# Performance work log

Measured on AMD Instinct MI355X. Metric: run time of the kernel, lower is better.

The kernel has to match this reference:

```python
import jax, jax.numpy as jnp
import numpy as np

GROUPS = 8   # GroupNorm groups used by create_pat_conv*_blocks(..., groups=8)
EPS = 1e-5
K = 20       # num_neighbor


def group_norm(x, gamma, beta):
    # x: [B, C, ...spatial]
    B, C = x.shape[0], x.shape[1]
    shape = x.shape
    xg = x.reshape(B, GROUPS, C // GROUPS, -1)
    m = xg.mean(axis=(2, 3), keepdims=True)
    v = ((xg - m) ** 2).mean(axis=(2, 3), keepdims=True)
    xg = (xg - m) * jax.lax.rsqrt(v + EPS)
    x = xg.reshape(shape)
    bshape = (1, C) + (1,) * (len(shape) - 2)
    return x * gamma.reshape(bshape) + beta.reshape(bshape)


def conv_block(x, w, b, gamma, beta):
    # pointwise (kernel-size 1) conv + GroupNorm + ELU, works for 1d and 2d spatial
    y = jnp.einsum('oc,bc...->bo...', w, x) + b.reshape((1, -1) + (1,) * (x.ndim - 2))
    return jax.nn.elu(group_norm(y, gamma, beta))


def knn_graph(points, k):
    # points: [B, 3, N] -> neighbor coords [B, 3, N, k] (self included, dilation=1)
    sq = jnp.sum(points * points, axis=1)                      # [B, N]
    inner = jnp.einsum('bci,bcj->bij', points, points)         # [B, N, N]
    dist = sq[:, :, None] + sq[:, None, :] - 2.0 * inner       # squared pairwise dist
    _, idx = jax.lax.top_k(-dist, k)                           # [B, N, k] smallest dists
    neighbors = jnp.take_along_axis(points[:, :, None, :], idx[:, None, :, :], axis=3)
    return neighbors                                           # [B, 3, N, k]


def setup_inputs() -> dict:
    key = jax.random.key(0)
    B, N = 4, 8192
    dims1 = [6, 32, 64]
    dims2 = [64, 512, 1024]
    keys = iter(jax.random.split(key, 32))
    inp = {"points": jax.random.normal(next(keys), (B, 3, N), dtype=jnp.float32)}
    for tag, dims in (("p1", dims1), ("p2", dims2)):
        for i in range(len(dims) - 1):
            cin, cout = dims[i], dims[i + 1]
            inp[f"{tag}_w{i}"] = jax.random.normal(next(keys), (cout, cin), dtype=jnp.float32) / np.float32(np.sqrt(cin))
            inp[f"{tag}_b{i}"] = jnp.zeros((cout,), dtype=jnp.float32)
            inp[f"{tag}_g{i}"] = jnp.ones((cout,), dtype=jnp.float32)
            inp[f"{tag}_beta{i}"] = jnp.zeros((cout,), dtype=jnp.float32)
    return inp


def reference(points, p1_w0, p1_b0, p1_g0, p1_beta0, p1_w1, p1_b1, p1_g1, p1_beta1,
              p2_w0, p2_b0, p2_g0, p2_beta0, p2_w1, p2_b1, p2_g1, p2_beta1):
    neighbors = knn_graph(points, K)                             # [B, 3, N, K]
    center = jnp.broadcast_to(points[:, :, :, None], neighbors.shape)
    x = jnp.concatenate([center, neighbors - center], axis=1)   # [B, 6, N, K]
    x = conv_block(x, p1_w0, p1_b0, p1_g0, p1_beta0)            # [B, 32, N, K]
    x = conv_block(x, p1_w1, p1_b1, p1_g1, p1_beta1)            # [B, 64, N, K]
    x = jnp.max(x, axis=2)                                      # [B, 64, K] (faithful to source: max over dim=2)
    x = conv_block(x, p2_w0, p2_b0, p2_g0, p2_beta0)            # [B, 512, K]
    x = conv_block(x, p2_w1, p2_b1, p2_g1, p2_beta1)            # [B, 1024, K]
    return x
```

## Files before the change

### kernel.cpp

```cpp
#include <hip/hip_runtime.h>
#include <math.h>

#define NPTS   8192
#define BATCH  4
#define KNN    20
#define NKTOT  (NPTS*KNN)
#define EPS    1e-5f
#define TILE2  2048

typedef float v2f __attribute__((ext_vector_type(2)));

__device__ __forceinline__ float elu(float x) { return x > 0.0f ? x : expm1f(x); }
__device__ __forceinline__ float eluf(float x) { return x > 0.0f ? x : __expf(x) - 1.0f; }
__device__ __forceinline__ v2f splat2(float x) { v2f v; v.x = x; v.y = x; return v; }
__device__ __forceinline__ float rfl(float x) {
    return __uint_as_float(__builtin_amdgcn_readfirstlane(__float_as_uint(x)));
}

__device__ __forceinline__ unsigned fenc(float f) {
    unsigned b = __float_as_uint(f);
    return b ^ ((unsigned)(((int)b) >> 31) | 0x80000000u);
}
__device__ __forceinline__ float fdec(unsigned u) {
    unsigned b = (u & 0x80000000u) ? (u ^ 0x80000000u) : ~u;
    return __uint_as_float(b);
}

__global__ __launch_bounds__(256) void prep_kernel(const float* __restrict__ points,
                                                   float4* __restrict__ pts4)
{
    const int t = blockIdx.x * 256 + threadIdx.x;
    const int b = t >> 13, n = t & (NPTS - 1);
    const float* px = points + b * 3 * NPTS;
    float x = px[n], y = px[NPTS + n], z = px[2 * NPTS + n];
    pts4[t] = make_float4(x, y, z, -0.5f * (x * x + y * y + z * z));
}

__global__ __launch_bounds__(256, 4) void knn_kernel(const float4* __restrict__ pts4,
                                                     int* __restrict__ idx_out)
{
    __shared__ __align__(16) float4 tileS[TILE2];
    const int tid  = threadIdx.x;
    const int lane = tid & 63;
    const int wv   = tid >> 6;
    const int b    = blockIdx.x >> 8;
    const int q0   = (blockIdx.x & 255) * 32 + wv * 8;
    const float4* pb = pts4 + b * NPTS;

    float qx[8], qy[8], qz[8];
    v2f smax2[8];
#pragma unroll
    for (int q = 0; q < 8; ++q) {
        float4 qp = pb[q0 + q];
        qx[q] = rfl(qp.x); qy[q] = rfl(qp.y); qz[q] = rfl(qp.z);
        smax2[q] = splat2(-INFINITY);
    }

    for (int t = 0; t < NPTS / TILE2; ++t) {
        __syncthreads();
        for (int i = tid; i < TILE2; i += 256) tileS[i] = pb[t * TILE2 + i];
        __syncthreads();
#pragma unroll 4
        for (int s = 0; s < TILE2 / 128; ++s) {
            float4 p0 = tileS[s * 128 + lane];
            float4 p1 = tileS[s * 128 + 64 + lane];
            v2f px = { p0.x, p1.x }, py = { p0.y, p1.y };
            v2f pz = { p0.z, p1.z }, pw = { p0.w, p1.w };
#pragma unroll
            for (int q = 0; q < 8; ++q) {
                v2f sv = __builtin_elementwise_fma(splat2(qx[q]), px,
                         __builtin_elementwise_fma(splat2(qy[q]), py,
                         __builtin_elementwise_fma(splat2(qz[q]), pz, pw)));
                smax2[q] = __builtin_elementwise_max(smax2[q], sv);
            }
        }
    }

    float sgate[8];
#pragma unroll
    for (int q = 0; q < 8; ++q) {
        float v = fmaxf(smax2[q].x, smax2[q].y);
#pragma unroll
        for (int k = 2; k <= 64; k <<= 1)
#pragma unroll
            for (int j = k >> 1; j >= 1; j >>= 1) {
                float o = __shfl_xor(v, j);
                bool up = ((lane & k) == 0);
                bool keepmin = (((lane & j) == 0) == up);
                v = keepmin ? fminf(v, o) : fmaxf(v, o);
            }
        float m = __shfl(v, 44);
        sgate[q] = m - 1e-4f - 1e-5f * fabsf(m);
    }

    float mys[8]; int myi[8]; float scur[8];
#pragma unroll
    for (int q = 0; q < 8; ++q) { mys[q] = -INFINITY; myi[q] = -1; scur[q] = -INFINITY; }

    for (int t = 0; t < NPTS / TILE2; ++t) {
        __syncthreads();
        for (int i = tid; i < TILE2; i += 256) tileS[i] = pb[t * TILE2 + i];
        __syncthreads();
        for (int s = 0; s < TILE2 / 128; ++s) {
            float4 p0 = tileS[s * 128 + lane];
            float4 p1 = tileS[s * 128 + 64 + lane];
            v2f px = { p0.x, p1.x }, py = { p0.y, p1.y };
            v2f pz = { p0.z, p1.z }, pw = { p0.w, p1.w };
            v2f sv2[8];
#pragma unroll
            for (int q = 0; q < 8; ++q)
                sv2[q] = __builtin_elementwise_fma(splat2(qx[q]), px,
                         __builtin_elementwise_fma(splat2(qy[q]), py,
                         __builtin_elementwise_fma(splat2(qz[q]), pz, pw)));
            const int jb = t * TILE2 + s * 128;
#pragma unroll
            for (int q = 0; q < 8; ++q) {
#pragma unroll
                for (int h = 0; h < 2; ++h) {
                    float svh = h ? sv2[q].y : sv2[q].x;
                    unsigned long long bal = __ballot(svh >= sgate[q]);
                    while (bal) {
                        int src = __ffsll(bal) - 1;
                        bal &= bal - 1;
                        float vs = __shfl(svh, src);
                        int   vi = jb + h * 64 + src;
                        if (vs > scur[q]) {
                            int   sh = (mys[q] < vs) ? 1 : 0;
                            float pd = __shfl_up(mys[q], 1);
                            int   pi = __shfl_up(myi[q], 1);
                            int   ps = __shfl_up(sh, 1);
                            bool pshift = (lane > 0) && (ps != 0);
                            mys[q] = sh ? (pshift ? pd : vs) : mys[q];
                            myi[q] = sh ? (pshift ? pi : vi) : myi[q];
                            scur[q] = __shfl(mys[q], 19);
                        }
                    }
                }
            }
        }
    }

#pragma unroll
    for (int q = 0; q < 8; ++q) {
        const int qi = q0 + q;
        if (lane < KNN) idx_out[(b * NPTS + qi) * KNN + lane] = myi[q];
    }
}

__global__ __launch_bounds__(256) void moments_x_kernel(const float* __restrict__ points,
                                                        const int* __restrict__ idx,
                                                        float* __restrict__ sums1p)
{
    const int t = blockIdx.x * 256 + threadIdx.x;
    const int b = blockIdx.x / 640;
    const int r = t - b * NKTOT;
    const int n = r / KNN;
    const float* px = points + b * 3 * NPTS;
    const int j = idx[t];
    float cx = px[n], cy = px[NPTS + n], cz = px[2 * NPTS + n];
    float v[27];
    v[0] = cx; v[1] = cy; v[2] = cz;
    v[3] = px[j] - cx; v[4] = px[NPTS + j] - cy; v[5] = px[2 * NPTS + j] - cz;
    int p = 6;
#pragma unroll
    for (int d = 0; d < 6; ++d)
#pragma unroll
        for (int e = d; e < 6; ++e) v[p++] = v[d] * v[e];
#pragma unroll
    for (int i = 0; i < 27; ++i)
        for (int o = 32; o > 0; o >>= 1) v[i] += __shfl_xor(v[i], o);

    __shared__ float red[4][27];
    const int lane = threadIdx.x & 63, w = threadIdx.x >> 6;
    if (lane == 0)
#pragma unroll
        for (int i = 0; i < 27; ++i) red[w][i] = v[i];
    __syncthreads();
    if (threadIdx.x < 27) {
        float acc = red[0][threadIdx.x] + red[1][threadIdx.x] + red[2][threadIdx.x] + red[3][threadIdx.x];
        int slot = blockIdx.x & 63;
        atomicAdd(&sums1p[(slot * BATCH + b) * 27 + threadIdx.x], acc);
    }
}

__global__ void finalize1_kernel(const float* __restrict__ sums1p,
                                 const float* __restrict__ w1, const float* __restrict__ b1,
                                 const float* __restrict__ g1, const float* __restrict__ beta1,
                                 float* __restrict__ w1f)
{
    __shared__ float S[BATCH][27];
    const int t = threadIdx.x;
    if (t < 108) {
        int b = t / 27, i = t % 27;
        float acc = 0.f;
        for (int s = 0; s < 64; ++s) acc += sums1p[(s * BATCH + b) * 27 + i];
        S[b][i] = acc;
    }
    __syncthreads();
    const int b = t >> 5, c = t & 31;
    const float invS = 1.0f / (float)NKTOT;
    float Ex[6], M[6][6];
#pragma unroll
    for (int d = 0; d < 6; ++d) Ex[d] = S[b][d] * invS;
    int p = 6;
#pragma unroll
    for (int d = 0; d < 6; ++d)
#pragma unroll
        for (int e = d; e < 6; ++e) { float v = S[b][p++] * invS; M[d][e] = v; M[e][d] = v; }
    const int g = c >> 2;
    float msum = 0.f, qsum = 0.f;
    for (int cc = g * 4; cc < g * 4 + 4; ++cc) {
        float w[6];
#pragma unroll
        for (int d = 0; d < 6; ++d) w[d] = w1[cc * 6 + d];
        float dotEx = 0.f;
#pragma unroll
        for (int d = 0; d < 6; ++d) dotEx += w[d] * Ex[d];
        float Ey = dotEx + b1[cc];
        float Ey2 = 0.f;
#pragma unroll
        for (int d = 0; d < 6; ++d)
#pragma unroll
            for (int e = 0; e < 6; ++e) Ey2 += w[d] * w[e] * M[d][e];
        Ey2 += 2.0f * b1[cc] * dotEx + b1[cc] * b1[cc];
        msum += Ey; qsum += Ey2;
    }
    float m = msum * 0.25f;
    float var = qsum * 0.25f - m * m;
    float inv = rsqrtf(var + EPS);
    float s = g1[c] * inv;
    float tt = s * (b1[c] - m) + beta1[c];
    float* o = w1f + (b * 32 + c) * 8;
#pragma unroll
    for (int d = 0; d < 6; ++d) o[d] = s * w1[c * 6 + d];
    o[6] = tt; o[7] = 0.f;
}

__global__ __launch_bounds__(256, 5) void fused_main_kernel(
    const float4* __restrict__ pts4, const int* __restrict__ idxb,
    const float* __restrict__ w1f, const float* __restrict__ w2, const float* __restrict__ b2,
    float* __restrict__ sums2p, unsigned int* __restrict__ maxenc, unsigned int* __restrict__ minenc)
{
    __shared__ __align__(16) float w2t[32 * 64];
    __shared__ __align__(16) float z1s[32 * 64];
    __shared__ __align__(16) float4 w1s4[64];
    __shared__ float b2s[64];
    __shared__ float redmx[64], redmn[64], sqred[32];

    const int t   = threadIdx.x;
    const int blk = blockIdx.x;
    const int nc  = blk & 15;
    const int k   = (blk >> 4) % 20;
    const int b   = blk / 320;

    for (int i = t; i < 512; i += 256) {
        float4 v = ((const float4*)w2)[i];
        int c = i >> 3, kq = (i & 7) * 4;
        w2t[(kq + 0) * 64 + c] = v.x; w2t[(kq + 1) * 64 + c] = v.y;
        w2t[(kq + 2) * 64 + c] = v.z; w2t[(kq + 3) * 64 + c] = v.w;
    }
    if (t < 64) { w1s4[t] = ((const float4*)w1f)[b * 64 + t]; b2s[t] = b2[t]; }

    const int ln   = t & 63;
    const int cg   = t >> 6;
    const int pos0 = (t & 15) * 4;
    const int c0   = (t >> 4) * 4;
    const float4* pb = pts4 + b * NPTS;
    const int nbase = nc * 512;

    float mx[4], mn[4];
#pragma unroll
    for (int ci = 0; ci < 4; ++ci) { mx[ci] = -INFINITY; mn[ci] = INFINITY; }
    float gs = 0.f, gq = 0.f;

    for (int st = 0; st < 8; ++st) {
        const int n = nbase + st * 64 + ln;
        const int j = idxb[(b * NPTS + n) * KNN + k];
        float4 c4 = pb[n];
        float4 e4 = pb[j];
        float x0[6] = { c4.x, c4.y, c4.z, e4.x - c4.x, e4.y - c4.y, e4.z - c4.z };

        __syncthreads();
#pragma unroll
        for (int jj = 0; jj < 8; ++jj) {
            int c = cg * 8 + jj;
            float4 wA = w1s4[c * 2 + 0];
            float4 wB = w1s4[c * 2 + 1];
            float z = wB.z;
            z = fmaf(wA.x, x0[0], z); z = fmaf(wA.y, x0[1], z); z = fmaf(wA.z, x0[2], z);
            z = fmaf(wA.w, x0[3], z); z = fmaf(wB.x, x0[4], z); z = fmaf(wB.y, x0[5], z);
            z1s[c * 64 + ln] = eluf(z);
        }
        __syncthreads();

        float acc[4][4];
#pragma unroll
        for (int ci = 0; ci < 4; ++ci) {
            float bb = b2s[c0 + ci];
#pragma unroll
            for (int pj = 0; pj < 4; ++pj) acc[ci][pj] = bb;
        }
#pragma unroll
        for (int kk = 0; kk < 32; ++kk) {
            float4 av = *(const float4*)&w2t[kk * 64 + c0];
            float4 bv = *(const float4*)&z1s[kk * 64 + pos0];
            float avv[4] = { av.x, av.y, av.z, av.w };
            float bvv[4] = { bv.x, bv.y, bv.z, bv.w };
#pragma unroll
            for (int ci = 0; ci < 4; ++ci)
#pragma unroll
                for (int pj = 0; pj < 4; ++pj) acc[ci][pj] = fmaf(avv[ci], bvv[pj], acc[ci][pj]);
        }
#pragma unroll
        for (int ci = 0; ci < 4; ++ci)
#pragma unroll
            for (int pj = 0; pj < 4; ++pj) {
                float v = acc[ci][pj];
                gs += v; gq = fmaf(v, v, gq);
                mx[ci] = fmaxf(mx[ci], v); mn[ci] = fminf(mn[ci], v);
            }
    }

#pragma unroll
    for (int m = 1; m <= 8; m <<= 1) {
#pragma unroll
        for (int ci = 0; ci < 4; ++ci) {
            mx[ci] = fmaxf(mx[ci], __shfl_xor(mx[ci], m));
            mn[ci] = fminf(mn[ci], __shfl_xor(mn[ci], m));
        }
        gs += __shfl_xor(gs, m);
        gq += __shfl_xor(gq, m);
    }
    if ((t & 15) == 0) {
        int qd = t >> 4;
#pragma unroll
        for (int ci = 0; ci < 4; ++ci) { redmx[qd * 4 + ci] = mx[ci]; redmn[qd * 4 + ci] = mn[ci]; }
        sqred[qd * 2 + 0] = gs; sqred[qd * 2 + 1] = gq;
    }
    __syncthreads();
    if (t < 64) {
        atomicMax(&maxenc[(b * 64 + t) * KNN + k], fenc(redmx[t]));
    } else if (t < 128) {
        int c = t - 64;
        atomicMin(&minenc[(b * 64 + c) * KNN + k], fenc(redmn[c]));
    } else if (t < 144) {
        int i2 = t - 128, g = i2 >> 1, w = i2 & 1;
        float v = sqred[(2 * g) * 2 + w] + sqred[(2 * g + 1) * 2 + w];
        int slot = blk & 63;
        atomicAdd(&sums2p[((slot * BATCH + b) * 8 + g) * 2 + w], v);
    }
}

__global__ void build_m1_kernel(const float* __restrict__ sums2p,
                                const unsigned int* __restrict__ maxenc,
                                const unsigned int* __restrict__ minenc,
                                const float* __restrict__ gamma, const float* __restrict__ beta,
                                float* __restrict__ m1)
{
    const int t = blockIdx.x * 256 + threadIdx.x;
    const int b = t / 1280;
    const int r = t - b * 1280;
    const int c = r / 20;
    const int g = c >> 3;
    float s = 0.f, q = 0.f;
    for (int sl = 0; sl < 64; ++sl) {
        s += sums2p[((sl * BATCH + b) * 8 + g) * 2 + 0];
        q += sums2p[((sl * BATCH + b) * 8 + g) * 2 + 1];
    }
    const float cnt = 8.0f * (float)NKTOT;
    float m = s / cnt;
    float var = q / cnt - m * m;
    float inv = rsqrtf(var + EPS);
    float sc = gamma[c] * inv;
    float tt = beta[c] - sc * m;
    float y = (sc >= 0.f) ? fdec(maxenc[t]) : fdec(minenc[t]);
    m1[t] = elu(sc * y + tt);
}

template <int CIN, int SLOTS>
__global__ void p2_gemm_kernel(const float* __restrict__ zin, const float* __restrict__ w,
                               const float* __restrict__ bias, float* __restrict__ yout,
                               float* __restrict__ sumsp, int chans_per_group)
{
    const int t = blockIdx.x * 256 + threadIdx.x;
    const int per_b = (gridDim.x * 256) / BATCH;
    const int b = t / per_b;
    const int r = t - b * per_b;
    const int o = r / 20;
    const int k = r - o * 20;
    const float* zb = zin + b * CIN * 20;
    const float* wrow = w + o * CIN;
    float acc = bias[o];
    for (int c = 0; c < CIN; c += 4) {
        float4 wv = *(const float4*)&wrow[c];
        acc += wv.x * zb[(c + 0) * 20 + k] + wv.y * zb[(c + 1) * 20 + k]
             + wv.z * zb[(c + 2) * 20 + k] + wv.w * zb[(c + 3) * 20 + k];
    }
    yout[t] = acc;

    __shared__ float ls[16];
    if (threadIdx.x < 16) ls[threadIdx.x] = 0.f;
    __syncthreads();
    const int g = o / chans_per_group;
    atomicAdd(&ls[g * 2 + 0], acc);
    atomicAdd(&ls[g * 2 + 1], acc * acc);
    __syncthreads();
    if (threadIdx.x < 16) {
        int slot = blockIdx.x & (SLOTS - 1);
        atomicAdd(&sumsp[(slot * BATCH + b) * 16 + threadIdx.x], ls[threadIdx.x]);
    }
}

template <int SLOTS>
__global__ void p2_finalize_kernel(const float* __restrict__ y, const float* __restrict__ sumsp,
                                   const float* __restrict__ gamma, const float* __restrict__ beta,
                                   float* __restrict__ z, int chans_per_group, float cnt)
{
    const int t = blockIdx.x * 256 + threadIdx.x;
    const int per_b = (gridDim.x * 256) / BATCH;
    const int b = t / per_b;
    const int r = t - b * per_b;
    const int o = r / 20;
    const int g = o / chans_per_group;
    float s = 0.f, q = 0.f;
    for (int sl = 0; sl < SLOTS; ++sl) {
        s += sumsp[(sl * BATCH + b) * 16 + g * 2 + 0];
        q += sumsp[(sl * BATCH + b) * 16 + g * 2 + 1];
    }
    float m = s / cnt;
    float var = q / cnt - m * m;
    float inv = rsqrtf(var + EPS);
    float v = gamma[o] * inv * (y[t] - m) + beta[o];
    z[t] = elu(v);
}

extern "C" void kernel_launch(void* const* d_in, const int* in_sizes, int n_in,
                              void* d_out, int out_size, void* d_ws, size_t ws_size,
                              hipStream_t stream)
{
    const float* points  = (const float*)d_in[0];
    const float* p1_w0   = (const float*)d_in[1];
    const float* p1_b0   = (const float*)d_in[2];
    const float* p1_g0   = (const float*)d_in[3];
    const float* p1_bt0  = (const float*)d_in[4];
    const float* p1_w1   = (const float*)d_in[5];
    const float* p1_b1   = (const float*)d_in[6];
    const float* p1_g1   = (const float*)d_in[7];
    const float* p1_bt1  = (const float*)d_in[8];
    const float* p2_w0   = (const float*)d_in[9];
    const float* p2_b0   = (const float*)d_in[10];
    const float* p2_g0   = (const float*)d_in[11];
    const float* p2_bt0  = (const float*)d_in[12];
    const float* p2_w1   = (const float*)d_in[13];
    const float* p2_b1   = (const float*)d_in[14];
    const float* p2_g1   = (const float*)d_in[15];
    const float* p2_bt1  = (const float*)d_in[16];
    float* out = (float*)d_out;

    float* ws = (float*)d_ws;
    int*      idx     = (int*)ws;
    float*    sums1p  = ws + 655360;
    float*    sums2p  = sums1p + 6912;
    float*    sumsAp  = sums2p + 4096;
    float*    sumsBp  = sumsAp + 1024;
    unsigned* maxenc  = (unsigned*)(sumsBp + 1024);
    unsigned* minenc  = maxenc + 5120;
    float*    w1f     = (float*)(minenc + 5120);
    float*    m1      = w1f + 1024;
    float*    yp2a    = m1 + 5120;
    float*    zp2a    = yp2a + 40960;
    float*    yp2b    = zp2a + 40960;
    float4*   pts4    = (float4*)yp2a;

    hipMemsetAsync(sums1p, 0, (6912 + 4096 + 1024 + 1024 + 5120) * sizeof(float), stream);
    hipMemsetAsync(minenc, 0xFF, 5120 * sizeof(unsigned), stream);

    prep_kernel<<<128, 256, 0, stream>>>(points, pts4);
    knn_kernel<<<1024, 256, 0, stream>>>(pts4, idx);
    moments_x_kernel<<<2560, 256, 0, stream>>>(points, idx, sums1p);
    finalize1_kernel<<<1, 128, 0, stream>>>(sums1p, p1_w0, p1_b0, p1_g0, p1_bt0, w1f);
    fused_main_kernel<<<1280, 256, 0, stream>>>(pts4, idx, w1f, p1_w1, p1_b1,
                                                sums2p, maxenc, minenc);
    build_m1_kernel<<<20, 256, 0, stream>>>(sums2p, maxenc, minenc, p1_g1, p1_bt1, m1);
    p2_gemm_kernel<64, 16><<<160, 256, 0, stream>>>(m1, p2_w0, p2_b0, yp2a, sumsAp, 64);
    p2_finalize_kernel<16><<<160, 256, 0, stream>>>(yp2a, sumsAp, p2_g0, p2_bt0, zp2a, 64, 1280.0f);
    p2_gemm_kernel<512, 16><<<320, 256, 0, stream>>>(zp2a, p2_w1, p2_b1, yp2b, sumsBp, 128);
    p2_finalize_kernel<16><<<320, 256, 0, stream>>>(yp2b, sumsBp, p2_g1, p2_bt1, out, 128, 2560.0f);
}
```

Before: 309.3 us.

## Replace serial warp top-k insertion with shared-memory candidate queue and bitonic sort

The second kNN pass no longer does a ballot-driven, wave-serial sorted insertion for each candidate that passes the gate. Each passing candidate now packs its encoded score and index into a 64-bit key and appends it to a per-query shared-memory queue with an atomic counter. After the pass, each wave runs a 64-wide bitonic sort on those keys and writes out the top 20. The shared tile shrinks to 1024 points to leave LDS room for the queues. Any candidates beyond the 64-slot cap are silently dropped, so results depend on the gate letting through no more than 64 points per query.

Result: faster. 296.6 us (-4.1%).

```diff
diff --git a/kernel.cpp b/kernel.cpp
--- a/kernel.cpp
+++ b/kernel.cpp
@@ -6,7 +6,8 @@
 #define KNN    20
 #define NKTOT  (NPTS*KNN)
 #define EPS    1e-5f
-#define TILE2  2048
+#define TILE3  1024
+#define QCAP   64
 
 typedef float v2f __attribute__((ext_vector_type(2)));
 
@@ -39,7 +40,10 @@
 __global__ __launch_bounds__(256, 4) void knn_kernel(const float4* __restrict__ pts4,
                                                      int* __restrict__ idx_out)
 {
-    __shared__ __align__(16) float4 tileS[TILE2];
+    __shared__ __align__(16) float4 tileS[TILE3];
+    __shared__ unsigned long long queue[32][QCAP];
+    __shared__ int qcnt[32];
+
     const int tid  = threadIdx.x;
     const int lane = tid & 63;
     const int wv   = tid >> 6;
@@ -55,13 +59,14 @@
         qx[q] = rfl(qp.x); qy[q] = rfl(qp.y); qz[q] = rfl(qp.z);
         smax2[q] = splat2(-INFINITY);
     }
-
-    for (int t = 0; t < NPTS / TILE2; ++t) {
-        __syncthreads();
-        for (int i = tid; i < TILE2; i += 256) tileS[i] = pb[t * TILE2 + i];
+    if (tid < 32) qcnt[tid] = 0;
+
+    for (int t = 0; t < NPTS / TILE3; ++t) {
+        __syncthreads();
+        for (int i = tid; i < TILE3; i += 256) tileS[i] = pb[t * TILE3 + i];
         __syncthreads();
 #pragma unroll 4
-        for (int s = 0; s < TILE2 / 128; ++s) {
+        for (int s = 0; s < TILE3 / 128; ++s) {
             float4 p0 = tileS[s * 128 + lane];
             float4 p1 = tileS[s * 128 + 64 + lane];
             v2f px = { p0.x, p1.x }, py = { p0.y, p1.y };
@@ -93,57 +98,56 @@
         sgate[q] = m - 1e-4f - 1e-5f * fabsf(m);
     }
 
-    float mys[8]; int myi[8]; float scur[8];
-#pragma unroll
-    for (int q = 0; q < 8; ++q) { mys[q] = -INFINITY; myi[q] = -1; scur[q] = -INFINITY; }
-
-    for (int t = 0; t < NPTS / TILE2; ++t) {
-        __syncthreads();
-        for (int i = tid; i < TILE2; i += 256) tileS[i] = pb[t * TILE2 + i];
-        __syncthreads();
-        for (int s = 0; s < TILE2 / 128; ++s) {
+    for (int t = 0; t < NPTS / TILE3; ++t) {
+        __syncthreads();
+        for (int i = tid; i < TILE3; i += 256) tileS[i] = pb[t * TILE3 + i];
+        __syncthreads();
+        for (int s = 0; s < TILE3 / 128; ++s) {
             float4 p0 = tileS[s * 128 + lane];
             float4 p1 = tileS[s * 128 + 64 + lane];
             v2f px = { p0.x, p1.x }, py = { p0.y, p1.y };
             v2f pz = { p0.z, p1.z }, pw = { p0.w, p1.w };
-            v2f sv2[8];
-#pragma unroll
-            for (int q = 0; q < 8; ++q)
-                sv2[q] = __builtin_elementwise_fma(splat2(qx[q]), px,
+            const int jb = t * TILE3 + s * 128;
+#pragma unroll
+            for (int q = 0; q < 8; ++q) {
+                v2f sv = __builtin_elementwise_fma(splat2(qx[q]), px,
                          __builtin_elementwise_fma(splat2(qy[q]), py,
                          __builtin_elementwise_fma(splat2(qz[q]), pz, pw)));
-            const int jb = t * TILE2 + s * 128;
-#pragma unroll
-            for (int q = 0; q < 8; ++q) {
 #pragma unroll
                 for (int h = 0; h < 2; ++h) {
-                    float svh = h ? sv2[q].y : sv2[q].x;
-                    unsigned long long bal = __ballot(svh >= sgate[q]);
-                    while (bal) {
-                        int src = __ffsll(bal) - 1;
-                        bal &= bal - 1;
-                        float vs = __shfl(svh, src);
-                        int   vi = jb + h * 64 + src;
-                        if (vs > scur[q]) {
-                            int   sh = (mys[q] < vs) ? 1 : 0;
-                            float pd = __shfl_up(mys[q], 1);
-                            int   pi = __shfl_up(myi[q], 1);
-                            int   ps = __shfl_up(sh, 1);
-                            bool pshift = (lane > 0) && (ps != 0);
-                            mys[q] = sh ? (pshift ? pd : vs) : mys[q];
-                            myi[q] = sh ? (pshift ? pi : vi) : myi[q];
-                            scur[q] = __shfl(mys[q], 19);
+                    float svh = h ? sv.y : sv.x;
+                    if (svh >= sgate[q]) {
+                        int slot = atomicAdd(&qcnt[wv * 8 + q], 1);
+                        if (slot < QCAP) {
+                            unsigned long long key =
+                                ((unsigned long long)fenc(svh) << 32)
+                                | (unsigned)(NPTS - 1 - (jb + h * 64 + lane));
+                            queue[wv * 8 + q][slot] = key;
                         }
                     }
                 }
             }
         }
     }
+    __syncthreads();
 
 #pragma unroll
     for (int q = 0; q < 8; ++q) {
-        const int qi = q0 + q;
-        if (lane < KNN) idx_out[(b * NPTS + qi) * KNN + lane] = myi[q];
+        const int cq = qcnt[wv * 8 + q];
+        unsigned long long key = (lane < cq) ? queue[wv * 8 + q][lane] : 0ull;
+#pragma unroll
+        for (int k = 2; k <= 64; k <<= 1)
+#pragma unroll
+            for (int j = k >> 1; j >= 1; j >>= 1) {
+                unsigned long long o = __shfl_xor(key, j);
+                bool up = ((lane & k) == 0);
+                bool keepmax = (((lane & j) == 0) == up);
+                bool omax = o > key;
+                key = (keepmax == omax) ? o : key;
+            }
+        if (lane < KNN)
+            idx_out[(b * NPTS + q0 + q) * KNN + lane] =
+                NPTS - 1 - (int)(unsigned)(key & 0xFFFFFFFFu);
     }
 }
 
```
